# Kernel tuning notes

Hardware: AMD Instinct MI355X
Metric: run time of the kernel (lower is better)

Reference implementation:

```python
import jax, jax.numpy as jnp
import numpy as np

N_NODES = 50000
N_EDGES = 800000
IN_FEATS = 1024
LAYERS = [128, 128]
EPS = 1e-5  # BatchNorm1d eps


def setup_inputs() -> dict:
    key = jax.random.key(0)
    ks = jax.random.split(key, 24)
    inp = {}
    inp["in_feat"] = jax.random.normal(ks[0], (N_NODES, IN_FEATS), jnp.float32)
    inp["src"] = jax.random.randint(ks[1], (N_EDGES,), 0, N_NODES, dtype=jnp.int32)
    inp["dst"] = jax.random.randint(ks[2], (N_EDGES,), 0, N_NODES, dtype=jnp.int32)
    dims = [IN_FEATS] + LAYERS
    i = 3
    for l in range(len(LAYERS)):
        din, dout = dims[l], dims[l + 1]
        s = 1.0 / np.sqrt(din)
        inp[f"W{l}"] = jax.random.uniform(ks[i], (din, dout), jnp.float32, -s, s); i += 1
        inp[f"b{l}"] = jnp.zeros((dout,), jnp.float32)
        inp[f"Wr{l}"] = jax.random.uniform(ks[i], (din, dout), jnp.float32, -s, s); i += 1
        inp[f"br{l}"] = jnp.zeros((dout,), jnp.float32)
        inp[f"gamma{l}"] = jnp.ones((dout,), jnp.float32)
        inp[f"beta{l}"] = jnp.zeros((dout,), jnp.float32)
        inp[f"mean{l}"] = jnp.zeros((dout,), jnp.float32)
        inp[f"var{l}"] = jnp.ones((dout,), jnp.float32)
    s = 1.0 / np.sqrt(LAYERS[-1])
    inp["Wd"] = jax.random.uniform(ks[i], (LAYERS[-1], 2), jnp.float32, -s, s)
    inp["bd"] = jnp.zeros((2,), jnp.float32)
    return inp


def gcn_layer(h, src, dst, W, b, Wr, br, gamma, beta, mean, var):
    # dgllife GCNLayer: GraphConv(norm='none', activation=relu) -> residual -> dropout(id, eval) -> BN(eval)
    msg = (h @ W)[src]                                        # [E, dout] gather of transformed src feats
    agg = jax.ops.segment_sum(msg, dst, num_segments=N_NODES)  # scatter-add to dst nodes
    new = jax.nn.relu(agg + b)                                 # GraphConv bias + activation
    res = jax.nn.relu(h @ Wr + br)                             # residual Linear + activation
    new = new + res
    return (new - mean) * jax.lax.rsqrt(var + EPS) * gamma + beta  # BatchNorm1d eval


def reference(in_feat, src, dst,
              W0, b0, Wr0, br0, gamma0, beta0, mean0, var0,
              W1, b1, Wr1, br1, gamma1, beta1, mean1, var1,
              Wd, bd):
    h = gcn_layer(in_feat, src, dst, W0, b0, Wr0, br0, gamma0, beta0, mean0, var0)
    h = gcn_layer(h, src, dst, W1, b1, Wr1, br1, gamma1, beta1, mean1, var1)
    logits = h @ Wd + bd                                       # [N, 2]
    return jax.nn.softmax(logits, axis=1)
```

## Files before the change

### kernel.cpp

```cpp
#include <hip/hip_runtime.h>
#include <math.h>

#define NNODES 50000
#define NEDGES 800000
#define KIN 1024
#define DH 128

typedef __bf16 bf16x8 __attribute__((ext_vector_type(8)));
typedef float floatx4 __attribute__((ext_vector_type(4)));

__global__ void k_zero2(int* __restrict__ a, int* __restrict__ b, int n) {
  int i = blockIdx.x * blockDim.x + threadIdx.x;
  if (i < n) { a[i] = 0; b[i] = 0; }
}

__global__ void k_hist(const int* __restrict__ dst, int* __restrict__ cnt, int E) {
  int i = blockIdx.x * blockDim.x + threadIdx.x;
  if (i < E) atomicAdd(&cnt[dst[i]], 1);
}

__global__ __launch_bounds__(1024) void k_scan_local(const int* __restrict__ cnt,
                                                     int* __restrict__ row_ptr,
                                                     int* __restrict__ bsum, int n) {
  __shared__ int sd[1024];
  int t = threadIdx.x;
  int i = blockIdx.x * 1024 + t;
  int v = (i < n) ? cnt[i] : 0;
  sd[t] = v;
  __syncthreads();
  for (int off = 1; off < 1024; off <<= 1) {
    int tv = (t >= off) ? sd[t - off] : 0;
    __syncthreads();
    sd[t] += tv;
    __syncthreads();
  }
  if (i < n) row_ptr[i] = sd[t] - v;
  if (t == 1023) bsum[blockIdx.x] = sd[t];
}

__global__ void k_scan_sums(const int* __restrict__ bsum, int* __restrict__ boff,
                            int nb, int* __restrict__ row_ptr, int n) {
  int lane = threadIdx.x;
  int v = (lane < nb) ? bsum[lane] : 0;
  int incl = v;
  for (int off = 1; off < 64; off <<= 1) {
    int t = __shfl_up(incl, off);
    if (lane >= off) incl += t;
  }
  boff[lane] = incl - v;
  if (lane == 63) row_ptr[n] = incl;
}

__global__ void k_scan_add(int* __restrict__ row_ptr, const int* __restrict__ boff, int n) {
  int i = blockIdx.x * blockDim.x + threadIdx.x;
  if (i < n) row_ptr[i] += boff[i >> 10];
}

__global__ void k_fill(const int* __restrict__ src, const int* __restrict__ dst,
                       const int* __restrict__ row_ptr, int* __restrict__ cursor,
                       int* __restrict__ csr_src, int E) {
  int i = blockIdx.x * blockDim.x + threadIdx.x;
  if (i < E) {
    int d = dst[i];
    int pos = row_ptr[d] + atomicAdd(&cursor[d], 1);
    csr_src[pos] = src[i];
  }
}

__global__ __launch_bounds__(256) void k_prepB(const float* __restrict__ W,
                                               const float* __restrict__ Wr,
                                               __bf16* __restrict__ Bt, int K, int kbits) {
  int id = blockIdx.x * 256 + threadIdx.x;
  int k = id & (K - 1);
  int n = id >> kbits;
  float v = (n < DH) ? W[(size_t)k * DH + n] : Wr[(size_t)k * DH + (n - DH)];
  Bt[(size_t)n * K + k] = (__bf16)v;
}

__device__ __forceinline__ void load_lds16(const void* g, void* l) {
  __builtin_amdgcn_global_load_lds(
      (const __attribute__((address_space(1))) unsigned int*)g,
      (__attribute__((address_space(3))) unsigned int*)l, 16, 0, 0);
}

template <typename AT, int K>
__global__ __launch_bounds__(256, 4) void k_gemm_mfma(
    const AT* __restrict__ X, const __bf16* __restrict__ Bt,
    const float* __restrict__ br, __bf16* __restrict__ XW,
    float* __restrict__ RES, int M) {
  __shared__ alignas(16) __bf16 As[32 * 72];
  __shared__ alignas(16) __bf16 Bs[256 * 64];
  const int tid = threadIdx.x;
  const int lane = tid & 63;
  const int w = tid >> 6;
  const int l15 = lane & 15;
  const int quad = lane >> 4;
  const int bm0 = blockIdx.x * 32;

  const int arow = tid >> 3;
  const int akq = (tid & 7) << 3;
  int agrow = bm0 + arow; if (agrow > M - 1) agrow = M - 1;
  const AT* aptr = X + (size_t)agrow * K + akq;

  floatx4 acc[2][4];
#pragma unroll
  for (int i = 0; i < 2; ++i)
#pragma unroll
    for (int j = 0; j < 4; ++j) acc[i][j] = (floatx4)0.f;

  for (int k0 = 0; k0 < K; k0 += 64) {
    if constexpr (sizeof(AT) == 4) {
      const float4 u = *(const float4*)(aptr + k0);
      const float4 v = *(const float4*)(aptr + k0 + 4);
      bf16x8 h;
      h[0] = (__bf16)u.x; h[1] = (__bf16)u.y; h[2] = (__bf16)u.z; h[3] = (__bf16)u.w;
      h[4] = (__bf16)v.x; h[5] = (__bf16)v.y; h[6] = (__bf16)v.z; h[7] = (__bf16)v.w;
      *(bf16x8*)&As[arow * 72 + akq] = h;
    } else {
      *(bf16x8*)&As[arow * 72 + akq] = *(const bf16x8*)(aptr + k0);
    }
#pragma unroll
    for (int ii = 0; ii < 8; ++ii) {
      const int wi = ii * 4 + w;
      const int n = wi * 8 + (lane >> 3);
      const int c = lane & 7;
      const int cs = c ^ (n & 7);
      const char* g = (const char*)Bt + (size_t)n * (K * 2) + (size_t)k0 * 2 + cs * 16;
      load_lds16(g, (char*)Bs + wi * 1024);
    }
    __syncthreads();
    bf16x8 af[2][2], bfr[4][2];
#pragma unroll
    for (int mt = 0; mt < 2; ++mt)
#pragma unroll
      for (int ks = 0; ks < 2; ++ks)
        af[mt][ks] = *(const bf16x8*)&As[(mt * 16 + l15) * 72 + ks * 32 + quad * 8];
#pragma unroll
    for (int nt = 0; nt < 4; ++nt) {
      const int n = w * 64 + nt * 16 + l15;
#pragma unroll
      for (int ks = 0; ks < 2; ++ks) {
        const int ch = (ks * 4 + quad) ^ (n & 7);
        bfr[nt][ks] = *(const bf16x8*)&Bs[n * 64 + ch * 8];
      }
    }
#pragma unroll
    for (int ks = 0; ks < 2; ++ks)
#pragma unroll
      for (int mt = 0; mt < 2; ++mt)
#pragma unroll
        for (int nt = 0; nt < 4; ++nt)
          acc[mt][nt] = __builtin_amdgcn_mfma_f32_16x16x32_bf16(af[mt][ks], bfr[nt][ks],
                                                                acc[mt][nt], 0, 0, 0);
    __syncthreads();
  }

  float* Cb = (float*)Bs;
#pragma unroll
  for (int mt = 0; mt < 2; ++mt)
#pragma unroll
    for (int nt = 0; nt < 4; ++nt)
#pragma unroll
      for (int r = 0; r < 4; ++r)
        Cb[(mt * 16 + quad * 4 + r) * 256 + (w * 64 + nt * 16 + l15)] = acc[mt][nt][r];
  __syncthreads();
  const int row = tid >> 3;
  const int seg = tid & 7;
  const int grow = bm0 + row;
  if (grow < M) {
    if (seg < 4) {
      const int c0 = seg * 32;
#pragma unroll
      for (int j = 0; j < 4; ++j) {
        const float4 v0 = *(const float4*)&Cb[row * 256 + c0 + j * 8];
        const float4 v1 = *(const float4*)&Cb[row * 256 + c0 + j * 8 + 4];
        bf16x8 h;
        h[0] = (__bf16)v0.x; h[1] = (__bf16)v0.y; h[2] = (__bf16)v0.z; h[3] = (__bf16)v0.w;
        h[4] = (__bf16)v1.x; h[5] = (__bf16)v1.y; h[6] = (__bf16)v1.z; h[7] = (__bf16)v1.w;
        *(bf16x8*)&XW[(size_t)grow * DH + c0 + j * 8] = h;
      }
    } else {
      const int c0 = (seg - 4) * 32;
#pragma unroll
      for (int j = 0; j < 8; ++j) {
        const float4 v = *(const float4*)&Cb[row * 256 + 128 + c0 + j * 4];
        const float4 bb = *(const float4*)&br[c0 + j * 4];
        *(float4*)&RES[(size_t)grow * DH + c0 + j * 4] =
            make_float4(fmaxf(v.x + bb.x, 0.f), fmaxf(v.y + bb.y, 0.f),
                        fmaxf(v.z + bb.z, 0.f), fmaxf(v.w + bb.w, 0.f));
      }
    }
  }
}

template <int MODE>
__global__ __launch_bounds__(256) void k_agg2(
    const __bf16* __restrict__ XW, const float* __restrict__ RES,
    const int* __restrict__ row_ptr, const int* __restrict__ csr_src,
    const float* __restrict__ b, const float* __restrict__ gamma,
    const float* __restrict__ beta, const float* __restrict__ mean,
    const float* __restrict__ var, const float* __restrict__ Wd,
    const float* __restrict__ bd, void* __restrict__ hout, int M) {
  const int node = (blockIdx.x << 2) + (threadIdx.x >> 6);
  const int lane = threadIdx.x & 63;
  if (node >= M) return;
  const int s = row_ptr[node], e = row_ptr[node + 1];
  const unsigned* xw = (const unsigned*)XW;
  float ax = 0.f, ay = 0.f;
  int i = s;
  for (; i + 3 < e; i += 4) {
    const int s0 = csr_src[i], s1 = csr_src[i + 1], s2 = csr_src[i + 2], s3 = csr_src[i + 3];
    const unsigned u0 = xw[(size_t)s0 * 64 + lane];
    const unsigned u1 = xw[(size_t)s1 * 64 + lane];
    const unsigned u2 = xw[(size_t)s2 * 64 + lane];
    const unsigned u3 = xw[(size_t)s3 * 64 + lane];
    ax += __uint_as_float(u0 << 16) + __uint_as_float(u1 << 16) +
          __uint_as_float(u2 << 16) + __uint_as_float(u3 << 16);
    ay += __uint_as_float(u0 & 0xffff0000u) + __uint_as_float(u1 & 0xffff0000u) +
          __uint_as_float(u2 & 0xffff0000u) + __uint_as_float(u3 & 0xffff0000u);
  }
  for (; i < e; ++i) {
    const unsigned u = xw[(size_t)csr_src[i] * 64 + lane];
    ax += __uint_as_float(u << 16);
    ay += __uint_as_float(u & 0xffff0000u);
  }
  const int f0 = lane << 1;
  const float2 bb = *(const float2*)&b[f0];
  const float2 rr = *(const float2*)&RES[(size_t)node * DH + f0];
  const float2 mm = *(const float2*)&mean[f0];
  const float2 vv = *(const float2*)&var[f0];
  const float2 gg = *(const float2*)&gamma[f0];
  const float2 be = *(const float2*)&beta[f0];
  const float x0 = fmaxf(ax + bb.x, 0.f) + rr.x;
  const float x1 = fmaxf(ay + bb.y, 0.f) + rr.y;
  const float y0 = (x0 - mm.x) * rsqrtf(vv.x + 1e-5f) * gg.x + be.x;
  const float y1 = (x1 - mm.y) * rsqrtf(vv.y + 1e-5f) * gg.y + be.y;
  if (MODE == 0) {
    union { __bf16 h[2]; unsigned u; } pk;
    pk.h[0] = (__bf16)y0;
    pk.h[1] = (__bf16)y1;
    ((unsigned*)hout)[(size_t)node * 64 + lane] = pk.u;
  } else {
    const float4 wv = *(const float4*)&Wd[f0 * 2];
    float l0 = y0 * wv.x + y1 * wv.z;
    float l1 = y0 * wv.y + y1 * wv.w;
#pragma unroll
    for (int off = 32; off > 0; off >>= 1) {
      l0 += __shfl_down(l0, off);
      l1 += __shfl_down(l1, off);
    }
    if (lane == 0) {
      l0 += bd[0];
      l1 += bd[1];
      const float m = fmaxf(l0, l1);
      const float e0 = expf(l0 - m), e1 = expf(l1 - m);
      const float inv = 1.f / (e0 + e1);
      float* out = (float*)hout;
      out[(size_t)node * 2] = e0 * inv;
      out[(size_t)node * 2 + 1] = e1 * inv;
    }
  }
}

extern "C" void kernel_launch(void* const* d_in, const int* in_sizes, int n_in,
                              void* d_out, int out_size, void* d_ws, size_t ws_size,
                              hipStream_t stream) {
  const float* in_feat = (const float*)d_in[0];
  const int* src = (const int*)d_in[1];
  const int* dst = (const int*)d_in[2];
  const float* W0 = (const float*)d_in[3];
  const float* b0 = (const float*)d_in[4];
  const float* Wr0 = (const float*)d_in[5];
  const float* br0 = (const float*)d_in[6];
  const float* gamma0 = (const float*)d_in[7];
  const float* beta0 = (const float*)d_in[8];
  const float* mean0 = (const float*)d_in[9];
  const float* var0 = (const float*)d_in[10];
  const float* W1 = (const float*)d_in[11];
  const float* b1 = (const float*)d_in[12];
  const float* Wr1 = (const float*)d_in[13];
  const float* br1 = (const float*)d_in[14];
  const float* gamma1 = (const float*)d_in[15];
  const float* beta1 = (const float*)d_in[16];
  const float* mean1 = (const float*)d_in[17];
  const float* var1 = (const float*)d_in[18];
  const float* Wd = (const float*)d_in[19];
  const float* bd = (const float*)d_in[20];
  float* out = (float*)d_out;

  char* ws = (char*)d_ws;
  size_t off = 0;
  auto alloc = [&](size_t bytes) {
    void* p = ws + off;
    off += (bytes + 255) & ~(size_t)255;
    return p;
  };
  __bf16* XWb = (__bf16*)alloc(sizeof(__bf16) * (size_t)NNODES * DH);
  __bf16* h1 = (__bf16*)alloc(sizeof(__bf16) * (size_t)NNODES * DH);
  float* RES = (float*)alloc(sizeof(float) * (size_t)NNODES * DH);
  int* cnt = (int*)alloc(sizeof(int) * NNODES);
  int* cursor = (int*)alloc(sizeof(int) * NNODES);
  int* row_ptr = (int*)alloc(sizeof(int) * (NNODES + 1));
  int* csr_src = (int*)alloc(sizeof(int) * NEDGES);
  int* bsum = (int*)alloc(sizeof(int) * 64);
  int* boff = (int*)alloc(sizeof(int) * 64);
  __bf16* Bt0 = (__bf16*)alloc(sizeof(__bf16) * 256 * KIN);
  __bf16* Bt1 = (__bf16*)alloc(sizeof(__bf16) * 256 * DH);

  const int nb = (NNODES + 1023) / 1024;
  k_zero2<<<(NNODES + 255) / 256, 256, 0, stream>>>(cnt, cursor, NNODES);
  k_hist<<<(NEDGES + 255) / 256, 256, 0, stream>>>(dst, cnt, NEDGES);
  k_scan_local<<<nb, 1024, 0, stream>>>(cnt, row_ptr, bsum, NNODES);
  k_scan_sums<<<1, 64, 0, stream>>>(bsum, boff, nb, row_ptr, NNODES);
  k_scan_add<<<(NNODES + 255) / 256, 256, 0, stream>>>(row_ptr, boff, NNODES);
  k_fill<<<(NEDGES + 255) / 256, 256, 0, stream>>>(src, dst, row_ptr, cursor, csr_src, NEDGES);

  k_prepB<<<KIN, 256, 0, stream>>>(W0, Wr0, Bt0, KIN, 10);
  k_prepB<<<DH, 256, 0, stream>>>(W1, Wr1, Bt1, DH, 7);

  const int ggrid = (NNODES + 31) / 32;
  const int agrid = (NNODES + 3) / 4;
  k_gemm_mfma<float, KIN><<<ggrid, 256, 0, stream>>>(in_feat, Bt0, br0, XWb, RES, NNODES);
  k_agg2<0><<<agrid, 256, 0, stream>>>(XWb, RES, row_ptr, csr_src, b0, gamma0, beta0,
                                       mean0, var0, nullptr, nullptr, h1, NNODES);
  k_gemm_mfma<__bf16, DH><<<ggrid, 256, 0, stream>>>(h1, Bt1, br1, XWb, RES, NNODES);
  k_agg2<1><<<agrid, 256, 0, stream>>>(XWb, RES, row_ptr, csr_src, b1, gamma1, beta1,
                                       mean1, var1, Wd, bd, out, NNODES);
}
```

Baseline: 558.3 us.

## Restructure GEMM with double-buffered async A staging and direct global B fragments

Reworks the MFMA GEMM to 64-row tiles and 512 threads arranged as 2x4 waves. The A tile (raw fp32 or bf16) is now loaded straight into LDS through double-buffered global_load_lds with an XOR swizzle, and converted to bf16 only when fragments are read. B fragments are read directly from global memory (expected to hit in cache) instead of being staged through LDS, which removes one barrier per k-step. The intent is to overlap the A fetch with compute and halve B traffic per row, at the cost of uncached-style global B reads inside the inner loop and an epilogue split into two halves.

```diff
diff --git a/kernel.cpp b/kernel.cpp
--- a/kernel.cpp
+++ b/kernel.cpp
@@ -84,112 +84,131 @@
 }
 
 template <typename AT, int K>
-__global__ __launch_bounds__(256, 4) void k_gemm_mfma(
+__global__ __launch_bounds__(512, 4) void k_gemm_mfma(
     const AT* __restrict__ X, const __bf16* __restrict__ Bt,
     const float* __restrict__ br, __bf16* __restrict__ XW,
     float* __restrict__ RES, int M) {
-  __shared__ alignas(16) __bf16 As[32 * 72];
-  __shared__ alignas(16) __bf16 Bs[256 * 64];
+  __shared__ alignas(16) char smem[32768];
   const int tid = threadIdx.x;
   const int lane = tid & 63;
   const int w = tid >> 6;
+  const int wr = w >> 2;
+  const int wc = w & 3;
   const int l15 = lane & 15;
   const int quad = lane >> 4;
-  const int bm0 = blockIdx.x * 32;
-
-  const int arow = tid >> 3;
-  const int akq = (tid & 7) << 3;
-  int agrow = bm0 + arow; if (agrow > M - 1) agrow = M - 1;
-  const AT* aptr = X + (size_t)agrow * K + akq;
-
-  floatx4 acc[2][4];
-#pragma unroll
-  for (int i = 0; i < 2; ++i)
-#pragma unroll
-    for (int j = 0; j < 4; ++j) acc[i][j] = (floatx4)0.f;
-
-  for (int k0 = 0; k0 < K; k0 += 64) {
+  const int bm0 = blockIdx.x * 64;
+  constexpr int ROWB = (sizeof(AT) == 4) ? 256 : 128;
+  constexpr int ABUF = 64 * ROWB;
+
+  auto stageA = [&](int buf, int k0) {
+    char* dst = smem + buf * ABUF;
     if constexpr (sizeof(AT) == 4) {
-      const float4 u = *(const float4*)(aptr + k0);
-      const float4 v = *(const float4*)(aptr + k0 + 4);
-      bf16x8 h;
-      h[0] = (__bf16)u.x; h[1] = (__bf16)u.y; h[2] = (__bf16)u.z; h[3] = (__bf16)u.w;
-      h[4] = (__bf16)v.x; h[5] = (__bf16)v.y; h[6] = (__bf16)v.z; h[7] = (__bf16)v.w;
-      *(bf16x8*)&As[arow * 72 + akq] = h;
-    } else {
-      *(bf16x8*)&As[arow * 72 + akq] = *(const bf16x8*)(aptr + k0);
-    }
-#pragma unroll
-    for (int ii = 0; ii < 8; ++ii) {
-      const int wi = ii * 4 + w;
-      const int n = wi * 8 + (lane >> 3);
-      const int c = lane & 7;
-      const int cs = c ^ (n & 7);
-      const char* g = (const char*)Bt + (size_t)n * (K * 2) + (size_t)k0 * 2 + cs * 16;
-      load_lds16(g, (char*)Bs + wi * 1024);
-    }
-    __syncthreads();
-    bf16x8 af[2][2], bfr[4][2];
-#pragma unroll
-    for (int mt = 0; mt < 2; ++mt)
-#pragma unroll
-      for (int ks = 0; ks < 2; ++ks)
-        af[mt][ks] = *(const bf16x8*)&As[(mt * 16 + l15) * 72 + ks * 32 + quad * 8];
-#pragma unroll
-    for (int nt = 0; nt < 4; ++nt) {
-      const int n = w * 64 + nt * 16 + l15;
-#pragma unroll
-      for (int ks = 0; ks < 2; ++ks) {
-        const int ch = (ks * 4 + quad) ^ (n & 7);
-        bfr[nt][ks] = *(const bf16x8*)&Bs[n * 64 + ch * 8];
-      }
-    }
-#pragma unroll
-    for (int ks = 0; ks < 2; ++ks)
-#pragma unroll
-      for (int mt = 0; mt < 2; ++mt)
-#pragma unroll
-        for (int nt = 0; nt < 4; ++nt)
-          acc[mt][nt] = __builtin_amdgcn_mfma_f32_16x16x32_bf16(af[mt][ks], bfr[nt][ks],
-                                                                acc[mt][nt], 0, 0, 0);
-    __syncthreads();
-  }
-
-  float* Cb = (float*)Bs;
-#pragma unroll
-  for (int mt = 0; mt < 2; ++mt)
-#pragma unroll
-    for (int nt = 0; nt < 4; ++nt)
-#pragma unroll
-      for (int r = 0; r < 4; ++r)
-        Cb[(mt * 16 + quad * 4 + r) * 256 + (w * 64 + nt * 16 + l15)] = acc[mt][nt][r];
-  __syncthreads();
-  const int row = tid >> 3;
-  const int seg = tid & 7;
-  const int grow = bm0 + row;
-  if (grow < M) {
-    if (seg < 4) {
-      const int c0 = seg * 32;
-#pragma unroll
-      for (int j = 0; j < 4; ++j) {
-        const float4 v0 = *(const float4*)&Cb[row * 256 + c0 + j * 8];
-        const float4 v1 = *(const float4*)&Cb[row * 256 + c0 + j * 8 + 4];
-        bf16x8 h;
-        h[0] = (__bf16)v0.x; h[1] = (__bf16)v0.y; h[2] = (__bf16)v0.z; h[3] = (__bf16)v0.w;
-        h[4] = (__bf16)v1.x; h[5] = (__bf16)v1.y; h[6] = (__bf16)v1.z; h[7] = (__bf16)v1.w;
-        *(bf16x8*)&XW[(size_t)grow * DH + c0 + j * 8] = h;
+#pragma unroll
+      for (int i = 0; i < 2; ++i) {
+        const int r = w * 8 + i * 4 + (lane >> 4);
+        int gr = bm0 + r; if (gr > M - 1) gr = M - 1;
+        const int c = (lane & 15) ^ (r & 7);
+        load_lds16((const char*)X + ((size_t)gr * K + k0 + c * 4) * 4,
+                   dst + (w * 8 + i * 4) * 256);
       }
     } else {
-      const int c0 = (seg - 4) * 32;
-#pragma unroll
-      for (int j = 0; j < 8; ++j) {
-        const float4 v = *(const float4*)&Cb[row * 256 + 128 + c0 + j * 4];
-        const float4 bb = *(const float4*)&br[c0 + j * 4];
-        *(float4*)&RES[(size_t)grow * DH + c0 + j * 4] =
-            make_float4(fmaxf(v.x + bb.x, 0.f), fmaxf(v.y + bb.y, 0.f),
-                        fmaxf(v.z + bb.z, 0.f), fmaxf(v.w + bb.w, 0.f));
+      const int r = w * 8 + (lane >> 3);
+      int gr = bm0 + r; if (gr > M - 1) gr = M - 1;
+      const int c = (lane & 7) ^ (r & 7);
+      load_lds16((const char*)X + ((size_t)gr * K + k0 + c * 8) * 2,
+                 dst + w * 8 * 128);
+    }
+  };
+
+  auto readA = [&](int buf, int mt, int ks) -> bf16x8 {
+    const int r = wr * 32 + mt * 16 + l15;
+    const char* rowp = smem + buf * ABUF + r * ROWB;
+    if constexpr (sizeof(AT) == 4) {
+      const int x = r & 7;
+      const int c0 = ks * 8 + quad * 2;
+      const floatx4 u = *(const floatx4*)(rowp + ((c0 ^ x) << 4));
+      const floatx4 v = *(const floatx4*)(rowp + (((c0 + 1) ^ x) << 4));
+      bf16x8 h;
+      h[0] = (__bf16)u[0]; h[1] = (__bf16)u[1]; h[2] = (__bf16)u[2]; h[3] = (__bf16)u[3];
+      h[4] = (__bf16)v[0]; h[5] = (__bf16)v[1]; h[6] = (__bf16)v[2]; h[7] = (__bf16)v[3];
+      return h;
+    } else {
+      const int cc = ks * 4 + quad;
+      return *(const bf16x8*)(rowp + ((cc ^ (r & 7)) << 4));
+    }
+  };
+
+  floatx4 acc[2][4];
+#pragma unroll
+  for (int i = 0; i < 2; ++i)
+#pragma unroll
+    for (int j = 0; j < 4; ++j) acc[i][j] = (floatx4)0.f;
+
+  stageA(0, 0);
+  __syncthreads();
+
+  constexpr int NS = K / 64;
+  for (int s = 0; s < NS; ++s) {
+    const int k0 = s * 64;
+    const int buf = s & 1;
+    if (s + 1 < NS) stageA(buf ^ 1, k0 + 64);
+#pragma unroll
+    for (int ks = 0; ks < 2; ++ks) {
+      const bf16x8 a0 = readA(buf, 0, ks);
+      const bf16x8 a1 = readA(buf, 1, ks);
+#pragma unroll
+      for (int nt = 0; nt < 4; ++nt) {
+        const int n = wc * 64 + nt * 16 + l15;
+        const bf16x8 bfrag =
+            *(const bf16x8*)(Bt + (size_t)n * K + k0 + ks * 32 + quad * 8);
+        acc[0][nt] = __builtin_amdgcn_mfma_f32_16x16x32_bf16(a0, bfrag, acc[0][nt], 0, 0, 0);
+        acc[1][nt] = __builtin_amdgcn_mfma_f32_16x16x32_bf16(a1, bfrag, acc[1][nt], 0, 0, 0);
       }
     }
+    __syncthreads();
+  }
+
+  float* Cb = (float*)smem;
+#pragma unroll
+  for (int half = 0; half < 2; ++half) {
+    if (wr == half) {
+#pragma unroll
+      for (int mt = 0; mt < 2; ++mt)
+#pragma unroll
+        for (int nt = 0; nt < 4; ++nt)
+#pragma unroll
+          for (int r = 0; r < 4; ++r)
+            Cb[(mt * 16 + quad * 4 + r) * 256 + wc * 64 + nt * 16 + l15] = acc[mt][nt][r];
+    }
+    __syncthreads();
+    const int row = tid >> 4;
+    const int seg = tid & 15;
+    const int grow = bm0 + half * 32 + row;
+    if (grow < M) {
+      if (seg < 8) {
+        const int c0 = seg * 16;
+#pragma unroll
+        for (int j = 0; j < 2; ++j) {
+          const float4 v0 = *(const float4*)&Cb[row * 256 + c0 + j * 8];
+          const float4 v1 = *(const float4*)&Cb[row * 256 + c0 + j * 8 + 4];
+          bf16x8 h;
+          h[0] = (__bf16)v0.x; h[1] = (__bf16)v0.y; h[2] = (__bf16)v0.z; h[3] = (__bf16)v0.w;
+          h[4] = (__bf16)v1.x; h[5] = (__bf16)v1.y; h[6] = (__bf16)v1.z; h[7] = (__bf16)v1.w;
+          *(bf16x8*)&XW[(size_t)grow * DH + c0 + j * 8] = h;
+        }
+      } else {
+        const int c0 = (seg - 8) * 16;
+#pragma unroll
+        for (int j = 0; j < 4; ++j) {
+          const float4 v = *(const float4*)&Cb[row * 256 + 128 + c0 + j * 4];
+          const float4 bb = *(const float4*)&br[c0 + j * 4];
+          *(float4*)&RES[(size_t)grow * DH + c0 + j * 4] =
+              make_float4(fmaxf(v.x + bb.x, 0.f), fmaxf(v.y + bb.y, 0.f),
+                          fmaxf(v.z + bb.z, 0.f), fmaxf(v.w + bb.w, 0.f));
+        }
+      }
+    }
+    __syncthreads();
   }
 }
 
@@ -318,12 +337,12 @@
   k_prepB<<<KIN, 256, 0, stream>>>(W0, Wr0, Bt0, KIN, 10);
   k_prepB<<<DH, 256, 0, stream>>>(W1, Wr1, Bt1, DH, 7);
 
-  const int ggrid = (NNODES + 31) / 32;
+  const int ggrid = (NNODES + 63) / 64;
   const int agrid = (NNODES + 3) / 4;
-  k_gemm_mfma<float, KIN><<<ggrid, 256, 0, stream>>>(in_feat, Bt0, br0, XWb, RES, NNODES);
+  k_gemm_mfma<float, KIN><<<ggrid, 512, 0, stream>>>(in_feat, Bt0, br0, XWb, RES, NNODES);
   k_agg2<0><<<agrid, 256, 0, stream>>>(XWb, RES, row_ptr, csr_src, b0, gamma0, beta0,
                                        mean0, var0, nullptr, nullptr, h1, NNODES);
-  k_gemm_mfma<__bf16, DH><<<ggrid, 256, 0, stream>>>(h1, Bt1, br1, XWb, RES, NNODES);
+  k_gemm_mfma<__bf16, DH><<<ggrid, 512, 0, stream>>>(h1, Bt1, br1, XWb, RES, NNODES);
   k_agg2<1><<<agrid, 256, 0, stream>>>(XWb, RES, row_ptr, csr_src, b1, gamma1, beta1,
                                        mean1, var1, Wd, bd, out, NNODES);
 }
```

Result: slower. 618.7 us (+10.8%).
